# Kernel tuning notes

Hardware: AMD Instinct MI355X
Metric: run time of the kernel (lower is better)

Reference implementation:

```python
import jax, jax.numpy as jnp
import numpy as np


def setup_inputs() -> dict:
    B, N, T, FH, FO = 4, 64, 64, 128, 64
    key = jax.random.key(0)
    k = jax.random.split(key, 5)
    h = jax.random.normal(k[0], (B, N, T, FH), dtype=jnp.float32)
    # fully-connected graph without self loops: E = N*(N-1)
    off = ~np.eye(N, dtype=bool)
    r_idx, s_idx = np.nonzero(off)          # receiver / sender node ids, [E]
    eye = np.eye(N, dtype=np.float32)
    rel_rec = jnp.asarray(eye[r_idx])       # [E, N] one-hot
    rel_send = jnp.asarray(eye[s_idx])      # [E, N] one-hot
    W_fc = jax.random.normal(k[1], (FO, FH), dtype=jnp.float32) * 0.1
    b_fc = jax.random.normal(k[2], (FO,), dtype=jnp.float32) * 0.1
    a_w = jax.random.normal(k[3], (1, 2 * FO), dtype=jnp.float32) * 0.05
    a_b = jax.random.normal(k[4], (1,), dtype=jnp.float32) * 0.05
    return {"h": h, "rel_rec": rel_rec, "rel_send": rel_send,
            "W_fc": W_fc, "b_fc": b_fc, "a_w": a_w, "a_b": a_b}


def reference(h, rel_rec, rel_send, W_fc, b_fc, a_w, a_b):
    B, N, T, _ = h.shape
    FO = W_fc.shape[0]
    # Wh = fc(h): [B, N, T, FO]
    Wh = jnp.einsum('bnth,oh->bnto', h, W_fc) + b_fc
    # one-hot matmul gather == direct indexing (selection matrices)
    ri = jnp.argmax(rel_rec, axis=1)   # [E] receiver node per edge
    si = jnp.argmax(rel_send, axis=1)  # [E] sender node per edge
    receivers = Wh[:, ri]              # [B, E, T, FO]
    senders = Wh[:, si]                # [B, E, T, FO]
    # a([recv, send]) split into two dot products (same math as concat+Linear)
    a_r, a_s = a_w[0, :FO], a_w[0, FO:]
    logits = jnp.einsum('beto,o->bet', receivers, a_r) \
           + jnp.einsum('beto,o->bet', senders, a_s) + a_b[0]
    edges_score = jnp.exp(jax.nn.leaky_relu(logits, negative_slope=0.2))  # [B, E, T]
    # rel_rec.T @ diag(score) @ rel_send == scatter score into A[recv, send]
    scores_t = edges_score.transpose(0, 2, 1)  # [B, T, E]
    A = jnp.zeros((B, T, N, N), dtype=Wh.dtype).at[:, :, ri, si].add(scores_t)
    A_sym = 0.5 * (A + A.swapaxes(-1, -2))
    A_norm = A / A.sum(-1, keepdims=True)
    Wh_t = Wh.transpose(0, 2, 1, 3)            # [B, T, N, FO]
    h_p = jax.nn.relu(jnp.matmul(A_norm, Wh_t)).transpose(0, 2, 1, 3)  # [B, N, T, FO]
    return h_p, A, A_sym, A_norm
```

## Files before the change

### kernel.cpp

```cpp
#include <hip/hip_runtime.h>
#include <stddef.h>

#define NN 64
#define TT 64
#define FHH 128
#define FOO 64

typedef float f4 __attribute__((ext_vector_type(4)));

__global__ __launch_bounds__(256) void gat_fused(
    const float* __restrict__ h,
    const float* __restrict__ Wfc,
    const float* __restrict__ bfc,
    const float* __restrict__ aw,
    const float* __restrict__ abp,
    float* __restrict__ out)
{
    __shared__ float h_lds[NN * 132];
    __shared__ float wT_lds[FHH * 68];
    __shared__ float wh_lds[NN * 68];
    __shared__ float A_lds[NN * 68];
    __shared__ float bias_lds[FOO], ar_lds[FOO], as_lds[FOO];
    __shared__ float rd_lds[NN], sd_lds[NN], inv_lds[NN];
    __shared__ float pr_lds[256], ps_lds[256];

    const int tid = threadIdx.x;
    const int b = blockIdx.x >> 6, t = blockIdx.x & 63;

    const f4* h4 = (const f4*)h;
#pragma unroll
    for (int i = 0; i < 8; ++i) {
        int idx = tid + 256 * i;
        int n = idx >> 5, k4 = idx & 31;
        f4 v = h4[(size_t)((b * NN + n) * TT + t) * (FHH / 4) + k4];
        *(f4*)&h_lds[n * 132 + k4 * 4] = v;
    }
    const f4* W4 = (const f4*)Wfc;
#pragma unroll
    for (int i = 0; i < 8; ++i) {
        int idx = tid + 256 * i;
        int o = idx & 63, k4 = idx >> 6;
        f4 v = W4[o * (FHH / 4) + k4];
#pragma unroll
        for (int kk = 0; kk < 4; ++kk)
            wT_lds[(k4 * 4 + kk) * 68 + o] = v[kk];
    }
    if (tid < FOO) {
        bias_lds[tid] = bfc[tid];
        ar_lds[tid]   = aw[tid];
        as_lds[tid]   = aw[FOO + tid];
    }
    const float ab = abp[0];
    __syncthreads();

    const int tx = tid & 15, ty = tid >> 4;
    const int o0 = tx * 4, r0 = ty * 4;

    float acc[4][4];
#pragma unroll
    for (int i2 = 0; i2 < 4; ++i2)
#pragma unroll
        for (int j = 0; j < 4; ++j) acc[i2][j] = 0.f;
#pragma unroll 4
    for (int kc = 0; kc < 32; ++kc) {
        f4 hv[4], wv[4];
#pragma unroll
        for (int i2 = 0; i2 < 4; ++i2) hv[i2] = *(const f4*)&h_lds[(r0 + i2) * 132 + kc * 4];
#pragma unroll
        for (int kk = 0; kk < 4; ++kk) wv[kk] = *(const f4*)&wT_lds[(kc * 4 + kk) * 68 + o0];
#pragma unroll
        for (int i2 = 0; i2 < 4; ++i2)
#pragma unroll
            for (int kk = 0; kk < 4; ++kk)
#pragma unroll
                for (int j = 0; j < 4; ++j)
                    acc[i2][j] += hv[i2][kk] * wv[kk][j];
    }
#pragma unroll
    for (int i2 = 0; i2 < 4; ++i2) {
        f4 v;
#pragma unroll
        for (int j = 0; j < 4; ++j) v[j] = acc[i2][j] + bias_lds[o0 + j];
        *(f4*)&wh_lds[(r0 + i2) * 68 + o0] = v;
    }
    __syncthreads();

    {
        int n = tid & 63, q = tid >> 6;
        float pr = 0.f, ps = 0.f;
#pragma unroll
        for (int c = 0; c < 4; ++c) {
            f4 v = *(const f4*)&wh_lds[n * 68 + q * 16 + c * 4];
#pragma unroll
            for (int j = 0; j < 4; ++j) {
                pr += v[j] * ar_lds[q * 16 + c * 4 + j];
                ps += v[j] * as_lds[q * 16 + c * 4 + j];
            }
        }
        pr_lds[q * 64 + n] = pr;
        ps_lds[q * 64 + n] = ps;
    }
    __syncthreads();
    if (tid < NN) {
        rd_lds[tid] = pr_lds[tid] + pr_lds[64 + tid] + pr_lds[128 + tid] + pr_lds[192 + tid];
        sd_lds[tid] = ps_lds[tid] + ps_lds[64 + tid] + ps_lds[128 + tid] + ps_lds[192 + tid];
    }
    __syncthreads();

    const size_t pageA = (size_t)blockIdx.x * (NN * NN);
    float* outA  = out + 1048576 + pageA;
    float* outAs = out + 2097152 + pageA;
    float* outAn = out + 3145728 + pageA;

#pragma unroll
    for (int i = 0; i < 16; ++i) {
        int idx = tid + 256 * i;
        int r = idx >> 6, s = idx & 63;
        float a = 0.f;
        if (r != s) {
            float lg = rd_lds[r] + sd_lds[s] + ab;
            float lr = lg > 0.f ? lg : 0.2f * lg;
            a = expf(lr);
        }
        A_lds[r * 68 + s] = a;
        outA[idx] = a;
    }
    __syncthreads();

    if (tid < NN) {
        float sum = 0.f;
#pragma unroll
        for (int c = 0; c < 16; ++c) {
            f4 v = *(const f4*)&A_lds[tid * 68 + c * 4];
            sum += v[0] + v[1] + v[2] + v[3];
        }
        inv_lds[tid] = 1.f / sum;
    }
    __syncthreads();

    float anv[16];
#pragma unroll
    for (int i = 0; i < 16; ++i) {
        int idx = tid + 256 * i;
        int r = idx >> 6, s = idx & 63;
        float a  = A_lds[r * 68 + s];
        float at = A_lds[s * 68 + r];
        outAs[idx] = 0.5f * (a + at);
        anv[i] = a * inv_lds[r];
        outAn[idx] = anv[i];
    }
    __syncthreads();
#pragma unroll
    for (int i = 0; i < 16; ++i) {
        int idx = tid + 256 * i;
        A_lds[(idx >> 6) * 68 + (idx & 63)] = anv[i];
    }
    __syncthreads();

#pragma unroll
    for (int i2 = 0; i2 < 4; ++i2)
#pragma unroll
        for (int j = 0; j < 4; ++j) acc[i2][j] = 0.f;
#pragma unroll 4
    for (int kc = 0; kc < 16; ++kc) {
        f4 av[4], wv[4];
#pragma unroll
        for (int i2 = 0; i2 < 4; ++i2) av[i2] = *(const f4*)&A_lds[(r0 + i2) * 68 + kc * 4];
#pragma unroll
        for (int kk = 0; kk < 4; ++kk) wv[kk] = *(const f4*)&wh_lds[(kc * 4 + kk) * 68 + o0];
#pragma unroll
        for (int i2 = 0; i2 < 4; ++i2)
#pragma unroll
            for (int kk = 0; kk < 4; ++kk)
#pragma unroll
                for (int j = 0; j < 4; ++j)
                    acc[i2][j] += av[i2][kk] * wv[kk][j];
    }
#pragma unroll
    for (int i2 = 0; i2 < 4; ++i2) {
        int r = r0 + i2;
        f4 v;
#pragma unroll
        for (int j = 0; j < 4; ++j) {
            float x = acc[i2][j];
            v[j] = x > 0.f ? x : 0.f;
        }
        *(f4*)&out[(size_t)((b * NN + r) * TT + t) * FOO + o0] = v;
    }
}

extern "C" void kernel_launch(void* const* d_in, const int* in_sizes, int n_in,
                              void* d_out, int out_size, void* d_ws, size_t ws_size,
                              hipStream_t stream) {
    const float* h   = (const float*)d_in[0];
    const float* Wfc = (const float*)d_in[3];
    const float* bfc = (const float*)d_in[4];
    const float* aw  = (const float*)d_in[5];
    const float* abp = (const float*)d_in[6];
    float* out = (float*)d_out;

    gat_fused<<<dim3(256), dim3(256), 0, stream>>>(h, Wfc, bfc, aw, abp, out);
}
```

Before: 86.65 us.

## Raise block size to 1024 threads with 2x2 register tiles per thread

```diff
diff --git a/kernel.cpp b/kernel.cpp
--- a/kernel.cpp
+++ b/kernel.cpp
@@ -7,8 +7,9 @@
 #define FOO 64
 
 typedef float f4 __attribute__((ext_vector_type(4)));
-
-__global__ __launch_bounds__(256) void gat_fused(
+typedef float f2 __attribute__((ext_vector_type(2)));
+
+__global__ __launch_bounds__(1024) void gat_fused(
     const float* __restrict__ h,
     const float* __restrict__ Wfc,
     const float* __restrict__ bfc,
@@ -22,23 +23,23 @@
     __shared__ float A_lds[NN * 68];
     __shared__ float bias_lds[FOO], ar_lds[FOO], as_lds[FOO];
     __shared__ float rd_lds[NN], sd_lds[NN], inv_lds[NN];
-    __shared__ float pr_lds[256], ps_lds[256];
+    __shared__ float pr_lds[16 * 64], ps_lds[16 * 64];
 
     const int tid = threadIdx.x;
     const int b = blockIdx.x >> 6, t = blockIdx.x & 63;
 
     const f4* h4 = (const f4*)h;
 #pragma unroll
-    for (int i = 0; i < 8; ++i) {
-        int idx = tid + 256 * i;
+    for (int i = 0; i < 2; ++i) {
+        int idx = tid + 1024 * i;
         int n = idx >> 5, k4 = idx & 31;
         f4 v = h4[(size_t)((b * NN + n) * TT + t) * (FHH / 4) + k4];
         *(f4*)&h_lds[n * 132 + k4 * 4] = v;
     }
     const f4* W4 = (const f4*)Wfc;
 #pragma unroll
-    for (int i = 0; i < 8; ++i) {
-        int idx = tid + 256 * i;
+    for (int i = 0; i < 2; ++i) {
+        int idx = tid + 1024 * i;
         int o = idx & 63, k4 = idx >> 6;
         f4 v = W4[o * (FHH / 4) + k4];
 #pragma unroll
@@ -53,57 +54,60 @@
     const float ab = abp[0];
     __syncthreads();
 
-    const int tx = tid & 15, ty = tid >> 4;
-    const int o0 = tx * 4, r0 = ty * 4;
-
-    float acc[4][4];
-#pragma unroll
-    for (int i2 = 0; i2 < 4; ++i2)
-#pragma unroll
-        for (int j = 0; j < 4; ++j) acc[i2][j] = 0.f;
-#pragma unroll 4
+    const int tx = tid & 31, ty = tid >> 5;
+    const int o0 = tx * 2, r0 = ty * 2;
+
+    float acc[2][2];
+#pragma unroll
+    for (int i2 = 0; i2 < 2; ++i2)
+#pragma unroll
+        for (int j = 0; j < 2; ++j) acc[i2][j] = 0.f;
+#pragma unroll 8
     for (int kc = 0; kc < 32; ++kc) {
-        f4 hv[4], wv[4];
-#pragma unroll
-        for (int i2 = 0; i2 < 4; ++i2) hv[i2] = *(const f4*)&h_lds[(r0 + i2) * 132 + kc * 4];
-#pragma unroll
-        for (int kk = 0; kk < 4; ++kk) wv[kk] = *(const f4*)&wT_lds[(kc * 4 + kk) * 68 + o0];
-#pragma unroll
-        for (int i2 = 0; i2 < 4; ++i2)
+        f4 hv[2]; f2 wv[4];
+#pragma unroll
+        for (int i2 = 0; i2 < 2; ++i2) hv[i2] = *(const f4*)&h_lds[(r0 + i2) * 132 + kc * 4];
+#pragma unroll
+        for (int kk = 0; kk < 4; ++kk) wv[kk] = *(const f2*)&wT_lds[(kc * 4 + kk) * 68 + o0];
+#pragma unroll
+        for (int i2 = 0; i2 < 2; ++i2)
 #pragma unroll
             for (int kk = 0; kk < 4; ++kk)
 #pragma unroll
-                for (int j = 0; j < 4; ++j)
+                for (int j = 0; j < 2; ++j)
                     acc[i2][j] += hv[i2][kk] * wv[kk][j];
     }
 #pragma unroll
-    for (int i2 = 0; i2 < 4; ++i2) {
-        f4 v;
-#pragma unroll
-        for (int j = 0; j < 4; ++j) v[j] = acc[i2][j] + bias_lds[o0 + j];
-        *(f4*)&wh_lds[(r0 + i2) * 68 + o0] = v;
+    for (int i2 = 0; i2 < 2; ++i2) {
+        f2 v;
+#pragma unroll
+        for (int j = 0; j < 2; ++j) v[j] = acc[i2][j] + bias_lds[o0 + j];
+        *(f2*)&wh_lds[(r0 + i2) * 68 + o0] = v;
     }
     __syncthreads();
 
     {
         int n = tid & 63, q = tid >> 6;
+        f4 v = *(const f4*)&wh_lds[n * 68 + q * 4];
         float pr = 0.f, ps = 0.f;
 #pragma unroll
-        for (int c = 0; c < 4; ++c) {
-            f4 v = *(const f4*)&wh_lds[n * 68 + q * 16 + c * 4];
-#pragma unroll
-            for (int j = 0; j < 4; ++j) {
-                pr += v[j] * ar_lds[q * 16 + c * 4 + j];
-                ps += v[j] * as_lds[q * 16 + c * 4 + j];
-            }
+        for (int j = 0; j < 4; ++j) {
+            pr += v[j] * ar_lds[q * 4 + j];
+            ps += v[j] * as_lds[q * 4 + j];
         }
         pr_lds[q * 64 + n] = pr;
         ps_lds[q * 64 + n] = ps;
     }
     __syncthreads();
     if (tid < NN) {
-        rd_lds[tid] = pr_lds[tid] + pr_lds[64 + tid] + pr_lds[128 + tid] + pr_lds[192 + tid];
-        sd_lds[tid] = ps_lds[tid] + ps_lds[64 + tid] + ps_lds[128 + tid] + ps_lds[192 + tid];
+        float r = 0.f, s = 0.f;
+#pragma unroll
+        for (int q = 0; q < 16; ++q) {
+            r += pr_lds[q * 64 + tid];
+            s += ps_lds[q * 64 + tid];
+        }
+        rd_lds[tid] = r;
+        sd_lds[tid] = s;
     }
     __syncthreads();
 
@@ -113,14 +117,14 @@
     float* outAn = out + 3145728 + pageA;
 
 #pragma unroll
-    for (int i = 0; i < 16; ++i) {
-        int idx = tid + 256 * i;
+    for (int i = 0; i < 4; ++i) {
+        int idx = tid + 1024 * i;
         int r = idx >> 6, s = idx & 63;
         float a = 0.f;
         if (r != s) {
             float lg = rd_lds[r] + sd_lds[s] + ab;
             float lr = lg > 0.f ? lg : 0.2f * lg;
-            a = expf(lr);
+            a = __expf(lr);
         }
         A_lds[r * 68 + s] = a;
         outA[idx] = a;
@@ -138,10 +142,10 @@
     }
     __syncthreads();
 
-    float anv[16];
-#pragma unroll
-    for (int i = 0; i < 16; ++i) {
-        int idx = tid + 256 * i;
+    float anv[4];
+#pragma unroll
+    for (int i = 0; i < 4; ++i) {
+        int idx = tid + 1024 * i;
         int r = idx >> 6, s = idx & 63;
         float a  = A_lds[r * 68 + s];
         float at = A_lds[s * 68 + r];
@@ -151,41 +155,41 @@
     }
     __syncthreads();
 #pragma unroll
-    for (int i = 0; i < 16; ++i) {
-        int idx = tid + 256 * i;
+    for (int i = 0; i < 4; ++i) {
+        int idx = tid + 1024 * i;
         A_lds[(idx >> 6) * 68 + (idx & 63)] = anv[i];
     }
     __syncthreads();
 
 #pragma unroll
-    for (int i2 = 0; i2 < 4; ++i2)
-#pragma unroll
-        for (int j = 0; j < 4; ++j) acc[i2][j] = 0.f;
-#pragma unroll 4
+    for (int i2 = 0; i2 < 2; ++i2)
+#pragma unroll
+        for (int j = 0; j < 2; ++j) acc[i2][j] = 0.f;
+#pragma unroll 8
     for (int kc = 0; kc < 16; ++kc) {
-        f4 av[4], wv[4];
-#pragma unroll
-        for (int i2 = 0; i2 < 4; ++i2) av[i2] = *(const f4*)&A_lds[(r0 + i2) * 68 + kc * 4];
-#pragma unroll
-        for (int kk = 0; kk < 4; ++kk) wv[kk] = *(const f4*)&wh_lds[(kc * 4 + kk) * 68 + o0];
-#pragma unroll
-        for (int i2 = 0; i2 < 4; ++i2)
+        f4 av[2]; f2 wv[4];
+#pragma unroll
+        for (int i2 = 0; i2 < 2; ++i2) av[i2] = *(const f4*)&A_lds[(r0 + i2) * 68 + kc * 4];
+#pragma unroll
+        for (int kk = 0; kk < 4; ++kk) wv[kk] = *(const f2*)&wh_lds[(kc * 4 + kk) * 68 + o0];
+#pragma unroll
+        for (int i2 = 0; i2 < 2; ++i2)
 #pragma unroll
             for (int kk = 0; kk < 4; ++kk)
 #pragma unroll
-                for (int j = 0; j < 4; ++j)
+                for (int j = 0; j < 2; ++j)
                     acc[i2][j] += av[i2][kk] * wv[kk][j];
     }
 #pragma unroll
-    for (int i2 = 0; i2 < 4; ++i2) {
+    for (int i2 = 0; i2 < 2; ++i2) {
         int r = r0 + i2;
-        f4 v;
-#pragma unroll
-        for (int j = 0; j < 4; ++j) {
+        f2 v;
+#pragma unroll
+        for (int j = 0; j < 2; ++j) {
             float x = acc[i2][j];
             v[j] = x > 0.f ? x : 0.f;
         }
-        *(f4*)&out[(size_t)((b * NN + r) * TT + t) * FOO + o0] = v;
+        *(f2*)&out[(size_t)((b * NN + r) * TT + t) * FOO + o0] = v;
     }
 }
 
@@ -199,5 +203,5 @@
     const float* abp = (const float*)d_in[6];
     float* out = (float*)d_out;
 
-    gat_fused<<<dim3(256), dim3(256), 0, stream>>>(h, Wfc, bfc, aw, abp, out);
+    gat_fused<<<dim3(256), dim3(1024), 0, stream>>>(h, Wfc, bfc, aw, abp, out);
 }
```

Measured after the change: 86.10 us. Within noise of the previous version (-0.6%).
